# Kernel optimization log

Measured on AMD Instinct MI355X. Metric: run time of the kernel, lower is better.

## Reference

```python
import jax, jax.numpy as jnp
import numpy as np

K = 4            # number of modes (init kwarg)
ALPHA = 2000.0   # bandwidth constraint
TAU = 0.0        # dual ascent step (0 -> exact reconstruction slack)
N_ITERS = 20     # fixed ADMM iterations (orig: tol-based while loop, max 500)


def vmd_batch(x):
    # x: [B, C, T] float32 -> (u: [B, C, K, T], omega: [B, C, K])
    B, C, T = x.shape
    T2 = 2 * T
    half = T2 // 2
    # mirror extension (vmdpy): flip first half | signal | flip second half
    f = jnp.concatenate([x[..., :T // 2][..., ::-1], x, x[..., T // 2:][..., ::-1]], axis=-1)  # [B,C,T2]
    t = jnp.arange(1, T2 + 1, dtype=jnp.float32) / T2
    freqs = t - 0.5 - 1.0 / T2                       # [T2], centered frequency axis
    freqs_pos = freqs[half:]                          # [T], positive frequencies
    f_hat = jnp.fft.fftshift(jnp.fft.fft(f, axis=-1), axes=-1).astype(jnp.complex64)
    f_hat_plus = f_hat.at[..., :half].set(0.0)        # keep analytic (positive-freq) part
    # init=1: uniform initial center frequencies
    omega = jnp.broadcast_to((0.5 / K) * jnp.arange(K, dtype=jnp.float32), (B, C, K))
    u_hat = jnp.zeros((B, C, K, T2), dtype=jnp.complex64)
    lam = jnp.zeros((B, C, T2), dtype=jnp.complex64)  # dual variable lambda_hat

    def step(carry, _):
        u_hat, omega, lam = carry
        S = jnp.sum(u_hat, axis=2)                    # running sum of all modes [B,C,T2]
        new_u, new_w = [], []
        for k in range(K):                            # Gauss-Seidel sweep over K modes (K small, unrolled)
            S = S - u_hat[:, :, k]                    # sum of all other modes (updated ones included)
            denom = 1.0 + ALPHA * (freqs[None, None, :] - omega[:, :, k:k + 1]) ** 2
            uk = (f_hat_plus - S + lam / 2.0) / denom # Wiener-filter spectral update [B,C,T2]
            S = S + uk
            p = uk.real[..., half:] ** 2 + uk.imag[..., half:] ** 2  # power on positive freqs [B,C,T]
            wk = jnp.sum(freqs_pos * p, axis=-1) / jnp.sum(p, axis=-1)  # center-frequency re-estimate
            new_u.append(uk)
            new_w.append(wk)
        u_hat = jnp.stack(new_u, axis=2)
        omega = jnp.stack(new_w, axis=-1)
        lam = lam + TAU * (S - f_hat_plus)            # dual ascent (tau=0 -> no-op, kept for fidelity)
        return (u_hat, omega, lam), None

    (u_hat, omega, lam), _ = jax.lax.scan(step, (u_hat, omega, lam), None, length=N_ITERS)

    # reconstruct full conjugate-symmetric spectrum
    pos = u_hat[..., half:]                           # [B,C,K,T]
    full = jnp.zeros((B, C, K, T2), dtype=jnp.complex64)
    full = full.at[..., half:].set(pos)
    full = full.at[..., 1:half + 1].set(jnp.conj(pos)[..., ::-1])  # full[half-j] = conj(pos[j])
    full = full.at[..., 0].set(jnp.conj(full[..., -1]))
    u = jnp.real(jnp.fft.ifft(jnp.fft.ifftshift(full, axes=-1), axis=-1))  # [B,C,K,T2]
    u = u[..., T2 // 4: 3 * T2 // 4]                  # de-mirror: center T samples
    return u, omega


def setup_inputs() -> dict:
    key = jax.random.key(0)
    x = jax.random.normal(key, (16, 8192, 4), dtype=jnp.float32)  # [B, T, C]
    return {"x": x}


def reference(x):
    # module forward: permute [B,T,C] -> [B,C,T], run VMD, return u:[B,K,T,C], omega:[B,K]
    u, omega = vmd_batch(jnp.transpose(x, (0, 2, 1)))
    u = jnp.transpose(u, (0, 2, 3, 1))                # [B,K,T,C]
    omega_b = jnp.mean(omega, axis=1)                 # collapse channel dim -> [B,K]
    return (u, omega_b)
```

## Files before the change

### kernel.cpp

```cpp
#include <hip/hip_runtime.h>


#define HALF      8192
#define NH        8192
#define NTHREADS  1024
#define KMODES    4
#define NITERS    20
#define ALPHA_F   2000.0f
#define SQH       0.70710678118654752440f
#define SENTINEL  0xFFFFFFFFu

typedef __fp16 half2_t __attribute__((ext_vector_type(2)));
typedef float  v2f     __attribute__((ext_vector_type(2)));

__device__ __forceinline__ unsigned bitrev13(unsigned x) { return __brev(x) >> 19; }
__device__ __forceinline__ unsigned bitrev11(unsigned x) { return __brev(x) >> 21; }
__device__ __forceinline__ int pidx(int i) { return i + (i >> 4); }

__device__ __forceinline__ unsigned pack_h2(float a, float b) {
    half2_t h = __builtin_amdgcn_cvt_pkrtz(a, b);
    return __builtin_bit_cast(unsigned, h);
}
__device__ __forceinline__ v2f unpack_h2(unsigned u) {
    half2_t h = __builtin_bit_cast(half2_t, u);
    v2f r; r.x = (float)h.x; r.y = (float)h.y; return r;
}

__device__ __forceinline__ unsigned ic_load(const unsigned* p) {
    return __hip_atomic_load(p, __ATOMIC_RELAXED, __HIP_MEMORY_SCOPE_AGENT);
}
__device__ __forceinline__ void ic_store(unsigned* p, unsigned v) {
    __hip_atomic_store(p, v, __ATOMIC_RELAXED, __HIP_MEMORY_SCOPE_AGENT);
}
__device__ __forceinline__ unsigned long long ic_load64(const unsigned long long* p) {
    return __hip_atomic_load(p, __ATOMIC_RELAXED, __HIP_MEMORY_SCOPE_AGENT);
}
__device__ __forceinline__ void ic_store64(unsigned long long* p, unsigned long long v) {
    __hip_atomic_store(p, v, __ATOMIC_RELAXED, __HIP_MEMORY_SCOPE_AGENT);
}
__device__ __forceinline__ void store_plain(unsigned* p, unsigned v) {
    asm volatile("global_store_dword %0, %1, off" :: "v"(p), "v"(v) : "memory");
}
__device__ __forceinline__ unsigned load_sc0(const unsigned* p) {
    unsigned r;
    asm volatile("global_load_dword %0, %1, off sc0\n\t"
                 "s_waitcnt vmcnt(0)"
                 : "=v"(r) : "v"(p) : "memory");
    return r;
}

template <int CTRL>
__device__ __forceinline__ float dpp_add_step(float v) {
    int r = __builtin_amdgcn_update_dpp(0, __float_as_int(v), CTRL, 0xf, 0xf, true);
    return v + __int_as_float(r);
}
__device__ __forceinline__ float wave64_sum(float v) {
    v = dpp_add_step<0x111>(v);
    v = dpp_add_step<0x112>(v);
    v = dpp_add_step<0x114>(v);
    v = dpp_add_step<0x118>(v);
    v = dpp_add_step<0x142>(v);
    v = dpp_add_step<0x143>(v);
    return v;
}

__device__ __forceinline__ float2 cmul(float2 a, float wr, float wi) {
    return make_float2(a.x * wr - a.y * wi, a.x * wi + a.y * wr);
}
__device__ __forceinline__ float2 cadd(float2 a, float2 b) {
    return make_float2(a.x + b.x, a.y + b.y);
}
__device__ __forceinline__ float2 csub(float2 a, float2 b) {
    return make_float2(a.x - b.x, a.y - b.y);
}

template <bool INV>
__device__ __forceinline__ void fft_pass8_g(float2* A, int bf, int log2Q, float invL) {
    const int Q    = 1 << log2Q;
    const int j    = bf & (Q - 1);
    const int base = ((bf >> log2Q) << (log2Q + 3)) + j;

    float2 x[8];
    #pragma unroll
    for (int m = 0; m < 8; ++m) x[m] = A[pidx(base + m * Q)];

    float rev = (float)j * invL;
    float w1r = __builtin_amdgcn_cosf(rev);
    float w1i = INV ?  __builtin_amdgcn_sinf(rev)
                    : -__builtin_amdgcn_sinf(rev);
    float w2r = w1r * w1r - w1i * w1i, w2i = 2.0f * w1r * w1i;
    float w4r = w2r * w2r - w2i * w2i, w4i = 2.0f * w2r * w2i;
    float wsr, wsi;
    if (INV) { wsr = SQH * (w1r - w1i); wsi = SQH * (w1r + w1i); }
    else     { wsr = SQH * (w1r + w1i); wsi = SQH * (w1i - w1r); }
    float w1tr = INV ? -w1i : w1i,  w1ti = INV ? w1r : -w1r;
    float wstr = INV ? -wsi : wsi,  wsti = INV ? wsr : -wsr;
    float w2tr = INV ? -w2i : w2i,  w2ti = INV ? w2r : -w2r;

    float2 y0 = cadd(x[0], x[4]), y1 = cadd(x[1], x[5]);
    float2 y2 = cadd(x[2], x[6]), y3 = cadd(x[3], x[7]);
    float2 y4 = cmul(csub(x[0], x[4]), w1r, w1i);
    float2 y5 = cmul(csub(x[1], x[5]), wsr, wsi);
    float2 y6 = cmul(csub(x[2], x[6]), w1tr, w1ti);
    float2 y7 = cmul(csub(x[3], x[7]), wstr, wsti);

    float2 z0 = cadd(y0, y2), z2 = cmul(csub(y0, y2), w2r, w2i);
    float2 z1 = cadd(y1, y3), z3 = cmul(csub(y1, y3), w2tr, w2ti);
    float2 z4 = cadd(y4, y6), z6 = cmul(csub(y4, y6), w2r, w2i);
    float2 z5 = cadd(y5, y7), z7 = cmul(csub(y5, y7), w2tr, w2ti);

    A[pidx(base + 0 * Q)] = cadd(z0, z1);
    A[pidx(base + 1 * Q)] = cmul(csub(z0, z1), w4r, w4i);
    A[pidx(base + 2 * Q)] = cadd(z2, z3);
    A[pidx(base + 3 * Q)] = cmul(csub(z2, z3), w4r, w4i);
    A[pidx(base + 4 * Q)] = cadd(z4, z5);
    A[pidx(base + 5 * Q)] = cmul(csub(z4, z5), w4r, w4i);
    A[pidx(base + 6 * Q)] = cadd(z6, z7);
    A[pidx(base + 7 * Q)] = cmul(csub(z6, z7), w4r, w4i);
}
template <bool INV>
__device__ __forceinline__ void fft_pass8(float2* A, int tid, int t) {
    fft_pass8_g<INV>(A, tid, 10 - 3 * t, (float)(1 << (3 * t)) * (1.0f / 8192.0f));
}

__device__ __forceinline__ void fft_last2(float2* A, int tid) {
    #pragma unroll
    for (int u = 0; u < 4; ++u) {
        int t  = tid + u * NTHREADS;
        int i0 = 2 * t, i1 = 2 * t + 1;
        float2 a = A[pidx(i0)], b = A[pidx(i1)];
        A[pidx(i0)] = make_float2(a.x + b.x, a.y + b.y);
        A[pidx(i1)] = make_float2(a.x - b.x, a.y - b.y);
    }
}

__device__ __forceinline__ void fft2048_last4(float2* A, int g) {
    int i0 = 4 * g;
    float2 a0 = A[pidx(i0)], a1 = A[pidx(i0 + 1)];
    float2 a2 = A[pidx(i0 + 2)], a3 = A[pidx(i0 + 3)];
    float2 b0 = cadd(a0, a2), b1 = cadd(a1, a3);
    float2 b2 = csub(a0, a2);
    float2 d  = csub(a1, a3);
    float2 b3 = make_float2(d.y, -d.x);
    A[pidx(i0)]     = cadd(b0, b1);
    A[pidx(i0 + 1)] = csub(b0, b1);
    A[pidx(i0 + 2)] = cadd(b2, b3);
    A[pidx(i0 + 3)] = csub(b2, b3);
}

__device__ __forceinline__ int mirror_t(int i) {
    if (i < 4096)       return 4095 - i;
    else if (i < 12288) return i - 4096;
    else                return 20479 - i;
}

__global__ __launch_bounds__(NTHREADS) void vmd_fused(
    const float* __restrict__ x, unsigned* __restrict__ ws_u,
    unsigned* __restrict__ ws_omega, unsigned* __restrict__ ws_partf,
    unsigned* __restrict__ ws_parts, unsigned* __restrict__ ws_udone,
    unsigned* __restrict__ ws_yflag, unsigned long long* __restrict__ ws_Y,
    float* __restrict__ out)
{
    __shared__ float2 A[NH + (NH >> 4)];
    const int tid = threadIdx.x;
    const int bid = blockIdx.x;
    const int r8  = bid & 7;
    const int q   = (bid >> 3) & 3;
    const int a8  = bid >> 5;
    const int ch  = a8 * 8 + r8;
    const int b   = ch >> 2, c = ch & 3;
    const float* xb = x + (size_t)b * 8192 * 4 + c;

    for (int m = tid; m < 2048; m += NTHREADS) {
        int i0 = 8 * m + 2 * q;
        float re = xb[(size_t)mirror_t(i0) * 4];
        float im = xb[(size_t)mirror_t(i0 + 1) * 4];
        A[pidx(m)] = make_float2(re, im);
    }
    __syncthreads();
    for (int t = 0; t < 3; ++t) {
        if (tid < 256)
            fft_pass8_g<false>(A, tid, 8 - 3 * t,
                               (float)(1 << (3 * t)) * (1.0f / 2048.0f));
        __syncthreads();
    }
    if (tid < 512) fft2048_last4(A, tid);
    __syncthreads();

    float2 own0, own1;
    {
        unsigned long long* ydst = ws_Y + ((size_t)ch * 4 + q) * 2048;
        own0 = A[pidx((int)bitrev11((unsigned)tid))];
        own1 = A[pidx((int)bitrev11((unsigned)(tid + NTHREADS)))];
        ic_store64(ydst + tid,            __builtin_bit_cast(unsigned long long, own0));
        ic_store64(ydst + tid + NTHREADS, __builtin_bit_cast(unsigned long long, own1));
    }
    asm volatile("s_waitcnt vmcnt(0)" ::: "memory");
    __syncthreads();
    if (tid == 0) ic_store(ws_yflag + ch * 4 + q, 0u);
    if (tid < 4) {
        const unsigned* p = ws_yflag + ch * 4 + tid;
        for (;;) {
            unsigned w = ic_load(p);
            if (w != SENTINEL) break;
            __builtin_amdgcn_s_sleep(1);
        }
    }
    __syncthreads();

    {
        A[pidx((q << 11) + tid)]            = own0;
        A[pidx((q << 11) + tid + NTHREADS)] = own1;
        const unsigned long long* ysrc = ws_Y + (size_t)ch * 8192;
        unsigned long long yv[6];
        int ri[3], n = 0;
        #pragma unroll
        for (int r = 0; r < 4; ++r) if (r != q) ri[n++] = r;
        #pragma unroll
        for (int w = 0; w < 3; ++w) {
            yv[2 * w]     = ic_load64(ysrc + (ri[w] << 11) + tid);
            yv[2 * w + 1] = ic_load64(ysrc + (ri[w] << 11) + tid + NTHREADS);
        }
        #pragma unroll
        for (int w = 0; w < 3; ++w) {
            A[pidx((ri[w] << 11) + tid)]            = __builtin_bit_cast(float2, yv[2 * w]);
            A[pidx((ri[w] << 11) + tid + NTHREADS)] = __builtin_bit_cast(float2, yv[2 * w + 1]);
        }
    }
    __syncthreads();

    v2f R[2];
    #pragma unroll
    for (int u = 0; u < 2; ++u) {
        int jp  = tid + u * NTHREADS;
        int j   = (q << 11) + jp;
        int j2p = (2048 - jp) & 2047;
        float2 y0 = A[pidx(jp)];
        float2 y1 = A[pidx(2048 + jp)];
        float2 y2 = A[pidx(4096 + jp)];
        float2 y3 = A[pidx(6144 + jp)];
        float2 h0 = A[pidx(j2p)];
        float2 h1 = A[pidx(2048 + j2p)];
        float2 h2 = A[pidx(4096 + j2p)];
        float2 h3 = A[pidx(6144 + j2p)];
        float rev = (float)j * (1.0f / 8192.0f);
        float wr = __builtin_amdgcn_cosf(rev);
        float wi = -__builtin_amdgcn_sinf(rev);
        float w2r = wr * wr - wi * wi, w2i = 2.0f * wr * wi;
        float w3r = w2r * wr - w2i * wi, w3i = w2r * wi + w2i * wr;
        float2 zj = y0;
        zj.x += y1.x * wr  - y1.y * wi;  zj.y += y1.x * wi  + y1.y * wr;
        zj.x += y2.x * w2r - y2.y * w2i; zj.y += y2.x * w2i + y2.y * w2r;
        zj.x += y3.x * w3r - y3.y * w3i; zj.y += y3.x * w3i + y3.y * w3r;
        float2 zh = h0;
        zh.x += h1.x * wr  + h1.y * wi;  zh.y += -h1.x * wi  + h1.y * wr;
        zh.x += h2.x * w2r + h2.y * w2i; zh.y += -h2.x * w2i + h2.y * w2r;
        zh.x += h3.x * w3r + h3.y * w3i; zh.y += -h3.x * w3i + h3.y * w3r;
        float ex = 0.5f * (zj.x + zh.x);
        float ey = 0.5f * (zj.y - zh.y);
        float dx = 0.5f * (zj.x - zh.x);
        float dy = 0.5f * (zj.y + zh.y);
        float rev2 = (float)j * (1.0f / 16384.0f);
        float ur = __builtin_amdgcn_cosf(rev2);
        float ui = -__builtin_amdgcn_sinf(rev2);
        R[u].x = ex + ur * dy + ui * dx;
        R[u].y = ey + ui * dy - ur * dx;
    }
    __syncthreads();

    v2f Up[KMODES][2];
    #pragma unroll
    for (int u = 0; u < 2; ++u)
        #pragma unroll
        for (int k = 0; k < KMODES; ++k) { Up[k][u].x = 0.f; Up[k][u].y = 0.f; }

    const float f0 = (float)((q << 11) + tid) * (1.0f / 16384.0f);
    float omg[KMODES] = {0.0f, 0.125f, 0.25f, 0.375f};

    float* red = (float*)A;
    const int lane = tid & 63, wid = tid >> 6;

    for (int it = 0; it < NITERS; ++it) {
        v2f nd[KMODES];
        #pragma unroll
        for (int k = 0; k < KMODES; ++k) { nd[k].x = 0.f; nd[k].y = 0.f; }
        #pragma unroll
        for (int u = 0; u < 2; ++u) {
            const float fru = f0 + (float)u * 0.0625f;
            v2f fv; fv.x = fru; fv.y = 1.0f;
            #pragma unroll
            for (int k = 0; k < KMODES; ++k) {
                float d   = fru - omg[k];
                float dnm = fmaf(ALPHA_F * d, d, 1.0f);
                float rcp = __builtin_amdgcn_rcpf(dnm);
                v2f uo  = Up[k][u];
                v2f nm  = R[u] + uo;
                v2f un  = nm * rcp;
                R[u]    = nm - un;
                Up[k][u] = un;
                float p = fmaf(un.x, un.x, un.y * un.y);
                nd[k]   = fv * p + nd[k];
            }
        }
        float num[KMODES], den[KMODES];
        #pragma unroll
        for (int m = 0; m < KMODES; ++m) {
            num[m] = wave64_sum(nd[m].x);
            den[m] = wave64_sum(nd[m].y);
        }
        float* redb = red + (it & 1) * 144;
        if (lane == 63) {
            float4* r4 = (float4*)&redb[wid * 8];
            r4[0] = make_float4(num[0], num[1], num[2], num[3]);
            r4[1] = make_float4(den[0], den[1], den[2], den[3]);
        }
        __syncthreads();
        const bool last_it = (it == NITERS - 1);
        unsigned* ppf = ws_partf + (((size_t)it * 64 + ch) << 5);
        unsigned* pps = ws_parts + (((size_t)it * 64 + ch) << 5);
        if (wid == 0) {
            float v = redb[lane] + redb[lane + 64];
            v += __int_as_float(__builtin_amdgcn_ds_swizzle(__float_as_int(v), 0x201F));
            v += __int_as_float(__builtin_amdgcn_ds_swizzle(__float_as_int(v), 0x401F));
            v += __int_as_float(__builtin_amdgcn_ds_bpermute((lane ^ 32) << 2,
                                                             __float_as_int(v)));
            if (lane < 8) {
                unsigned bits = __float_as_uint(v);
                store_plain(ppf + (q << 3) + lane, bits);
                ic_store(pps + (q << 3) + lane, bits);
            }
            if (!last_it || q == 0) {
                float t = 0.0f;
                if (lane < 32) {
                    unsigned w;
                    for (;;) {
                        w = load_sc0(ppf + lane);
                        if (w != SENTINEL) break;
                        w = ic_load(pps + lane);
                        if (w != SENTINEL) break;
                        __builtin_amdgcn_s_sleep(1);
                    }
                    t = __uint_as_float(w);
                }
                t += __int_as_float(__builtin_amdgcn_ds_swizzle(__float_as_int(t), 0x201F));
                t += __int_as_float(__builtin_amdgcn_ds_swizzle(__float_as_int(t), 0x401F));
                if (!last_it) {
                    if (lane < 8) redb[128 + lane] = t;
                } else {
                    #pragma unroll
                    for (int m = 0; m < KMODES; ++m) {
                        float nm_ = __int_as_float(__builtin_amdgcn_readlane(__float_as_int(t), m));
                        float dn_ = __int_as_float(__builtin_amdgcn_readlane(__float_as_int(t), m + 4));
                        omg[m] = nm_ * __builtin_amdgcn_rcpf(dn_);
                    }
                }
            }
        }
        if (!last_it) {
            __syncthreads();
            #pragma unroll
            for (int m = 0; m < KMODES; ++m) {
                float nm_ = redb[128 + m];
                float dn_ = redb[128 + m + 4];
                omg[m] = nm_ * __builtin_amdgcn_rcpf(dn_);
            }
        }
    }

    #pragma unroll
    for (int k = 0; k < KMODES; ++k) {
        unsigned* dst = ws_u + (size_t)(ch * KMODES + k) * HALF + (q << 11);
        #pragma unroll
        for (int u = 0; u < 2; ++u)
            ic_store(dst + tid + u * NTHREADS, pack_h2(Up[k][u].x, Up[k][u].y));
    }
    if (q == 0 && tid < KMODES)
        ic_store(ws_omega + ch * KMODES + tid, __float_as_uint(omg[tid]));
    asm volatile("s_waitcnt vmcnt(0)" ::: "memory");
    __syncthreads();
    if (tid == 0)
        ic_store(ws_udone + (ch << 2) + q, 0u);

    const int s2  = bid & 7;
    const int c2  = (bid >> 3) & 3;
    const int a2  = bid >> 5;
    const int g2  = a2 * 8 + s2;
    const int b2  = g2 >> 2, k2 = g2 & 3;
    const int ch2 = b2 * 4 + c2;
    const unsigned* pos = ws_u + (size_t)(ch2 * KMODES + k2) * HALF;

    if (bid == 0 && tid < 64) {
        int bb = tid >> 2, kk = tid & 3;
        float s = 0.f;
        #pragma unroll
        for (int cc = 0; cc < 4; ++cc) {
            const unsigned* p = ws_omega + ((bb * 4 + cc) << 2) + kk;
            unsigned w;
            for (;;) {
                w = ic_load(p);
                if (w != SENTINEL) break;
                __builtin_amdgcn_s_sleep(1);
            }
            s += __uint_as_float(w);
        }
        out[2097152 + tid] = 0.25f * s;
    }

    if (tid < 4) {
        const unsigned* p = ws_udone + (ch2 << 2) + tid;
        for (;;) {
            unsigned w = ic_load(p);
            if (w != SENTINEL) break;
            __builtin_amdgcn_s_sleep(1);
        }
    }
    __syncthreads();

    {
        unsigned wj[8], wh[8];
        #pragma unroll
        for (int uu = 0; uu < 8; ++uu) {
            int j = tid + uu * NTHREADS;
            wj[uu] = ic_load(pos + j);
            wh[uu] = ic_load(pos + (j ? (HALF - j) : (HALF - 1)));
        }
        #pragma unroll
        for (int uu = 0; uu < 8; ++uu) {
            int j = tid + uu * NTHREADS;
            v2f pj = unpack_h2(wj[uu]);
            v2f ph = unpack_h2(wh[uu]);
            float gjx = pj.x, gjy = (j == 0) ? -pj.y : pj.y;
            float ghx = ph.x, ghy = -ph.y;
            float ex = 0.5f * (gjx + ghx), ey = 0.5f * (gjy + ghy);
            float dx = 0.5f * (gjx - ghx), dy = 0.5f * (gjy - ghy);
            float rev = (float)j * (1.0f / 16384.0f);
            float wr = __builtin_amdgcn_cosf(rev);
            float wi = __builtin_amdgcn_sinf(rev);
            float ox = dx * wr - dy * wi;
            float oy = dx * wi + dy * wr;
            A[pidx(j)] = make_float2(ex - oy, ey + ox);
        }
    }
    __syncthreads();

    for (int t = 0; t < 4; ++t) {
        fft_pass8<true>(A, tid, t);
        __syncthreads();
    }
    fft_last2(A, tid);
    __syncthreads();

    float* outp = out + (size_t)(b2 * 4 + k2) * 8192 * 4 + c2;
    for (int m = 2048 + tid; m < 6144; m += NTHREADS) {
        float2 z = A[pidx((int)bitrev13((unsigned)m))];
        int t0 = 2 * m - 4096;
        outp[(size_t)t0 * 4]       = z.x * (1.0f / 8192.0f);
        outp[(size_t)(t0 + 1) * 4] = z.y * (1.0f / 8192.0f);
    }
}

extern "C" void kernel_launch(void* const* d_in, const int* in_sizes, int n_in,
                              void* d_out, int out_size, void* d_ws, size_t ws_size,
                              hipStream_t stream)
{
    (void)in_sizes; (void)n_in; (void)out_size; (void)ws_size;
    const float* x = (const float*)d_in[0];
    float* out = (float*)d_out;

    unsigned* ws_u     = (unsigned*)d_ws;
    unsigned* ws_omega = (unsigned*)((char*)d_ws + (size_t)64 * 4 * HALF * 4);
    unsigned* ws_partf = ws_omega + 256;
    unsigned* ws_parts = ws_partf + (size_t)NITERS * 64 * 32;
    unsigned* ws_udone = ws_parts + (size_t)NITERS * 64 * 32;
    unsigned* ws_yflag = ws_udone + 256;
    unsigned long long* ws_Y = (unsigned long long*)(ws_yflag + 256);

    hipMemsetAsync(ws_omega, 0xFF,
                   (size_t)(256 + 2 * NITERS * 64 * 32 + 256 + 256) * 4, stream);
    vmd_fused<<<256, NTHREADS, 0, stream>>>(x, ws_u, ws_omega, ws_partf,
                                            ws_parts, ws_udone, ws_yflag,
                                            ws_Y, out);
}
```

Before: 79.82 us.

## Interleave two channels per block to hide cross-block omega reduction latency

Each block now owns one octant of frequency bins for two different channels (A and B, offset by four octants) rather than a quarter of one channel. The ADMM loop alternates between them, so the global gather of channel B's partial sums from the previous iteration overlaps with channel A's local compute, and the reverse. The aim is to hide the inter-block spin-wait latency that previously stalled every iteration. The cost is a second Y-load and combine pass, doubled partial-sum and flag workspace, and more complex synchronisation ordering.

```diff
diff --git a/kernel.cpp b/kernel.cpp
--- a/kernel.cpp
+++ b/kernel.cpp
@@ -62,6 +62,32 @@
     v = dpp_add_step<0x142>(v);
     v = dpp_add_step<0x143>(v);
     return v;
+}
+
+__device__ __forceinline__ float fold16x8(const float* slab, int lane) {
+    float v = slab[lane] + slab[lane + 64];
+    v += __int_as_float(__builtin_amdgcn_ds_swizzle(__float_as_int(v), 0x201F));
+    v += __int_as_float(__builtin_amdgcn_ds_swizzle(__float_as_int(v), 0x401F));
+    v += __int_as_float(__builtin_amdgcn_ds_bpermute((lane ^ 32) << 2,
+                                                     __float_as_int(v)));
+    return v;
+}
+__device__ __forceinline__ float gather_fold(const unsigned* basef,
+                                             const unsigned* bases, int lane) {
+    unsigned w;
+    for (;;) {
+        w = load_sc0(basef + lane);
+        if (w != SENTINEL) break;
+        w = ic_load(bases + lane);
+        if (w != SENTINEL) break;
+        __builtin_amdgcn_s_sleep(1);
+    }
+    float t = __uint_as_float(w);
+    t += __int_as_float(__builtin_amdgcn_ds_swizzle(__float_as_int(t), 0x201F));
+    t += __int_as_float(__builtin_amdgcn_ds_swizzle(__float_as_int(t), 0x401F));
+    t += __int_as_float(__builtin_amdgcn_ds_bpermute((lane ^ 32) << 2,
+                                                     __float_as_int(t)));
+    return t;
 }
 
 __device__ __forceinline__ float2 cmul(float2 a, float wr, float wi) {
@@ -154,6 +180,43 @@
     else                return 20479 - i;
 }
 
+__device__ __forceinline__ v2f combine_bin(const float2* A, int j) {
+    int jp  = j & 2047;
+    int j2p = (2048 - jp) & 2047;
+    float2 y0 = A[pidx(jp)];
+    float2 y1 = A[pidx(2048 + jp)];
+    float2 y2 = A[pidx(4096 + jp)];
+    float2 y3 = A[pidx(6144 + jp)];
+    float2 h0 = A[pidx(j2p)];
+    float2 h1 = A[pidx(2048 + j2p)];
+    float2 h2 = A[pidx(4096 + j2p)];
+    float2 h3 = A[pidx(6144 + j2p)];
+    float rev = (float)j * (1.0f / 8192.0f);
+    float wr = __builtin_amdgcn_cosf(rev);
+    float wi = -__builtin_amdgcn_sinf(rev);
+    float w2r = wr * wr - wi * wi, w2i = 2.0f * wr * wi;
+    float w3r = w2r * wr - w2i * wi, w3i = w2r * wi + w2i * wr;
+    float2 zj = y0;
+    zj.x += y1.x * wr  - y1.y * wi;  zj.y += y1.x * wi  + y1.y * wr;
+    zj.x += y2.x * w2r - y2.y * w2i; zj.y += y2.x * w2i + y2.y * w2r;
+    zj.x += y3.x * w3r - y3.y * w3i; zj.y += y3.x * w3i + y3.y * w3r;
+    float2 zh = h0;
+    zh.x += h1.x * wr  + h1.y * wi;  zh.y += -h1.x * wi  + h1.y * wr;
+    zh.x += h2.x * w2r + h2.y * w2i; zh.y += -h2.x * w2i + h2.y * w2r;
+    zh.x += h3.x * w3r + h3.y * w3i; zh.y += -h3.x * w3i + h3.y * w3r;
+    float ex = 0.5f * (zj.x + zh.x);
+    float ey = 0.5f * (zj.y - zh.y);
+    float dx = 0.5f * (zj.x - zh.x);
+    float dy = 0.5f * (zj.y + zh.y);
+    float rev2 = (float)j * (1.0f / 16384.0f);
+    float ur = __builtin_amdgcn_cosf(rev2);
+    float ui = -__builtin_amdgcn_sinf(rev2);
+    v2f R;
+    R.x = ex + ur * dy + ui * dx;
+    R.y = ey + ui * dy - ur * dx;
+    return R;
+}
+
 __global__ __launch_bounds__(NTHREADS) void vmd_fused(
     const float* __restrict__ x, unsigned* __restrict__ ws_u,
     unsigned* __restrict__ ws_omega, unsigned* __restrict__ ws_partf,
@@ -162,17 +225,17 @@
     float* __restrict__ out)
 {
     __shared__ float2 A[NH + (NH >> 4)];
-    const int tid = threadIdx.x;
-    const int bid = blockIdx.x;
-    const int r8  = bid & 7;
-    const int q   = (bid >> 3) & 3;
-    const int a8  = bid >> 5;
-    const int ch  = a8 * 8 + r8;
-    const int b   = ch >> 2, c = ch & 3;
-    const float* xb = x + (size_t)b * 8192 * 4 + c;
+    const int tid  = threadIdx.x;
+    const int bid  = blockIdx.x;
+    const int chA  = bid & 63;
+    const int octA = bid >> 6;
+    const int chB  = chA ^ 1;
+    const int octB = octA + 4;
+    const int bA   = chA >> 2, cA = chA & 3;
+    const float* xb = x + (size_t)bA * 8192 * 4 + cA;
 
     for (int m = tid; m < 2048; m += NTHREADS) {
-        int i0 = 8 * m + 2 * q;
+        int i0 = 8 * m + 2 * octA;
         float re = xb[(size_t)mirror_t(i0) * 4];
         float im = xb[(size_t)mirror_t(i0 + 1) * 4];
         A[pidx(m)] = make_float2(re, im);
@@ -189,7 +252,7 @@
 
     float2 own0, own1;
     {
-        unsigned long long* ydst = ws_Y + ((size_t)ch * 4 + q) * 2048;
+        unsigned long long* ydst = ws_Y + ((size_t)chA * 4 + octA) * 2048;
         own0 = A[pidx((int)bitrev11((unsigned)tid))];
         own1 = A[pidx((int)bitrev11((unsigned)(tid + NTHREADS)))];
         ic_store64(ydst + tid,            __builtin_bit_cast(unsigned long long, own0));
@@ -197,9 +260,9 @@
     }
     asm volatile("s_waitcnt vmcnt(0)" ::: "memory");
     __syncthreads();
-    if (tid == 0) ic_store(ws_yflag + ch * 4 + q, 0u);
+    if (tid == 0) ic_store(ws_yflag + chA * 4 + octA, 0u);
     if (tid < 4) {
-        const unsigned* p = ws_yflag + ch * 4 + tid;
+        const unsigned* p = ws_yflag + chA * 4 + tid;
         for (;;) {
             unsigned w = ic_load(p);
             if (w != SENTINEL) break;
@@ -207,15 +270,14 @@
         }
     }
     __syncthreads();
-
     {
-        A[pidx((q << 11) + tid)]            = own0;
-        A[pidx((q << 11) + tid + NTHREADS)] = own1;
-        const unsigned long long* ysrc = ws_Y + (size_t)ch * 8192;
+        A[pidx((octA << 11) + tid)]            = own0;
+        A[pidx((octA << 11) + tid + NTHREADS)] = own1;
+        const unsigned long long* ysrc = ws_Y + (size_t)chA * 8192;
         unsigned long long yv[6];
         int ri[3], n = 0;
         #pragma unroll
-        for (int r = 0; r < 4; ++r) if (r != q) ri[n++] = r;
+        for (int r = 0; r < 4; ++r) if (r != octA) ri[n++] = r;
         #pragma unroll
         for (int w = 0; w < 3; ++w) {
             yv[2 * w]     = ic_load64(ysrc + (ri[w] << 11) + tid);
@@ -228,130 +290,156 @@
         }
     }
     __syncthreads();
-
-    v2f R[2];
+    v2f RA = combine_bin(A, (octA << 10) + tid);
+    __syncthreads();
+
+    if (tid < 4) {
+        const unsigned* p = ws_yflag + chB * 4 + tid;
+        for (;;) {
+            unsigned w = ic_load(p);
+            if (w != SENTINEL) break;
+            __builtin_amdgcn_s_sleep(1);
+        }
+    }
+    __syncthreads();
+    {
+        const unsigned long long* ysrc = ws_Y + (size_t)chB * 8192;
+        unsigned long long yv[8];
+        #pragma unroll
+        for (int r = 0; r < 4; ++r) {
+            yv[2 * r]     = ic_load64(ysrc + (r << 11) + tid);
+            yv[2 * r + 1] = ic_load64(ysrc + (r << 11) + tid + NTHREADS);
+        }
+        #pragma unroll
+        for (int r = 0; r < 4; ++r) {
+            A[pidx((r << 11) + tid)]            = __builtin_bit_cast(float2, yv[2 * r]);
+            A[pidx((r << 11) + tid + NTHREADS)] = __builtin_bit_cast(float2, yv[2 * r + 1]);
+        }
+    }
+    __syncthreads();
+    v2f RB = combine_bin(A, (octB << 10) + tid);
+    __syncthreads();
+
+    v2f UpA[KMODES], UpB[KMODES];
     #pragma unroll
-    for (int u = 0; u < 2; ++u) {
-        int jp  = tid + u * NTHREADS;
-        int j   = (q << 11) + jp;
-        int j2p = (2048 - jp) & 2047;
-        float2 y0 = A[pidx(jp)];
-        float2 y1 = A[pidx(2048 + jp)];
-        float2 y2 = A[pidx(4096 + jp)];
-        float2 y3 = A[pidx(6144 + jp)];
-        float2 h0 = A[pidx(j2p)];
-        float2 h1 = A[pidx(2048 + j2p)];
-        float2 h2 = A[pidx(4096 + j2p)];
-        float2 h3 = A[pidx(6144 + j2p)];
-        float rev = (float)j * (1.0f / 8192.0f);
-        float wr = __builtin_amdgcn_cosf(rev);
-        float wi = -__builtin_amdgcn_sinf(rev);
-        float w2r = wr * wr - wi * wi, w2i = 2.0f * wr * wi;
-        float w3r = w2r * wr - w2i * wi, w3i = w2r * wi + w2i * wr;
-        float2 zj = y0;
-        zj.x += y1.x * wr  - y1.y * wi;  zj.y += y1.x * wi  + y1.y * wr;
-        zj.x += y2.x * w2r - y2.y * w2i; zj.y += y2.x * w2i + y2.y * w2r;
-        zj.x += y3.x * w3r - y3.y * w3i; zj.y += y3.x * w3i + y3.y * w3r;
-        float2 zh = h0;
-        zh.x += h1.x * wr  + h1.y * wi;  zh.y += -h1.x * wi  + h1.y * wr;
-        zh.x += h2.x * w2r + h2.y * w2i; zh.y += -h2.x * w2i + h2.y * w2r;
-        zh.x += h3.x * w3r + h3.y * w3i; zh.y += -h3.x * w3i + h3.y * w3r;
-        float ex = 0.5f * (zj.x + zh.x);
-        float ey = 0.5f * (zj.y - zh.y);
-        float dx = 0.5f * (zj.x - zh.x);
-        float dy = 0.5f * (zj.y + zh.y);
-        float rev2 = (float)j * (1.0f / 16384.0f);
-        float ur = __builtin_amdgcn_cosf(rev2);
-        float ui = -__builtin_amdgcn_sinf(rev2);
-        R[u].x = ex + ur * dy + ui * dx;
-        R[u].y = ey + ui * dy - ur * dx;
-    }
-    __syncthreads();
-
-    v2f Up[KMODES][2];
-    #pragma unroll
-    for (int u = 0; u < 2; ++u)
-        #pragma unroll
-        for (int k = 0; k < KMODES; ++k) { Up[k][u].x = 0.f; Up[k][u].y = 0.f; }
-
-    const float f0 = (float)((q << 11) + tid) * (1.0f / 16384.0f);
-    float omg[KMODES] = {0.0f, 0.125f, 0.25f, 0.375f};
-
-    float* red = (float*)A;
+    for (int k = 0; k < KMODES; ++k) {
+        UpA[k].x = 0.f; UpA[k].y = 0.f;
+        UpB[k].x = 0.f; UpB[k].y = 0.f;
+    }
+    float omgA[KMODES] = {0.0f, 0.125f, 0.25f, 0.375f};
+    float omgB[KMODES] = {0.0f, 0.125f, 0.25f, 0.375f};
+    const float fA = (float)((octA << 10) + tid) * (1.0f / 16384.0f);
+    const float fB = (float)((octB << 10) + tid) * (1.0f / 16384.0f);
+
+    float* slabA  = (float*)A;
+    float* oslabA = slabA + 128;
+    float* slabB  = slabA + 136;
+    float* oslabB = slabA + 264;
     const int lane = tid & 63, wid = tid >> 6;
 
     for (int it = 0; it < NITERS; ++it) {
-        v2f nd[KMODES];
-        #pragma unroll
-        for (int k = 0; k < KMODES; ++k) { nd[k].x = 0.f; nd[k].y = 0.f; }
-        #pragma unroll
-        for (int u = 0; u < 2; ++u) {
-            const float fru = f0 + (float)u * 0.0625f;
-            v2f fv; fv.x = fru; fv.y = 1.0f;
+        const bool last_it = (it == NITERS - 1);
+        {
+            v2f nd[KMODES];
+            #pragma unroll
+            for (int k = 0; k < KMODES; ++k) { nd[k].x = 0.f; nd[k].y = 0.f; }
+            v2f fv; fv.x = fA; fv.y = 1.0f;
             #pragma unroll
             for (int k = 0; k < KMODES; ++k) {
-                float d   = fru - omg[k];
+                float d   = fA - omgA[k];
                 float dnm = fmaf(ALPHA_F * d, d, 1.0f);
                 float rcp = __builtin_amdgcn_rcpf(dnm);
-                v2f uo  = Up[k][u];
-                v2f nm  = R[u] + uo;
-                v2f un  = nm * rcp;
-                R[u]    = nm - un;
-                Up[k][u] = un;
+                v2f nm = RA + UpA[k];
+                v2f un = nm * rcp;
+                RA = nm - un;
+                UpA[k] = un;
                 float p = fmaf(un.x, un.x, un.y * un.y);
-                nd[k]   = fv * p + nd[k];
-            }
-        }
-        float num[KMODES], den[KMODES];
-        #pragma unroll
-        for (int m = 0; m < KMODES; ++m) {
-            num[m] = wave64_sum(nd[m].x);
-            den[m] = wave64_sum(nd[m].y);
-        }
-        float* redb = red + (it & 1) * 144;
-        if (lane == 63) {
-            float4* r4 = (float4*)&redb[wid * 8];
-            r4[0] = make_float4(num[0], num[1], num[2], num[3]);
-            r4[1] = make_float4(den[0], den[1], den[2], den[3]);
+                nd[k] = fv * p + nd[k];
+            }
+            float num[KMODES], den[KMODES];
+            #pragma unroll
+            for (int m = 0; m < KMODES; ++m) {
+                num[m] = wave64_sum(nd[m].x);
+                den[m] = wave64_sum(nd[m].y);
+            }
+            if (lane == 63) {
+                float4* r4 = (float4*)&slabA[wid * 8];
+                r4[0] = make_float4(num[0], num[1], num[2], num[3]);
+                r4[1] = make_float4(den[0], den[1], den[2], den[3]);
+            }
         }
         __syncthreads();
-        const bool last_it = (it == NITERS - 1);
-        unsigned* ppf = ws_partf + (((size_t)it * 64 + ch) << 5);
-        unsigned* pps = ws_parts + (((size_t)it * 64 + ch) << 5);
+        unsigned* pAf = ws_partf + (((size_t)it * 64 + chA) << 6);
+        unsigned* pAs = ws_parts + (((size_t)it * 64 + chA) << 6);
         if (wid == 0) {
-            float v = redb[lane] + redb[lane + 64];
-            v += __int_as_float(__builtin_amdgcn_ds_swizzle(__float_as_int(v), 0x201F));
-            v += __int_as_float(__builtin_amdgcn_ds_swizzle(__float_as_int(v), 0x401F));
-            v += __int_as_float(__builtin_amdgcn_ds_bpermute((lane ^ 32) << 2,
-                                                             __float_as_int(v)));
+            float v = fold16x8(slabA, lane);
             if (lane < 8) {
                 unsigned bits = __float_as_uint(v);
-                store_plain(ppf + (q << 3) + lane, bits);
-                ic_store(pps + (q << 3) + lane, bits);
-            }
-            if (!last_it || q == 0) {
-                float t = 0.0f;
-                if (lane < 32) {
-                    unsigned w;
-                    for (;;) {
-                        w = load_sc0(ppf + lane);
-                        if (w != SENTINEL) break;
-                        w = ic_load(pps + lane);
-                        if (w != SENTINEL) break;
-                        __builtin_amdgcn_s_sleep(1);
-                    }
-                    t = __uint_as_float(w);
-                }
-                t += __int_as_float(__builtin_amdgcn_ds_swizzle(__float_as_int(t), 0x201F));
-                t += __int_as_float(__builtin_amdgcn_ds_swizzle(__float_as_int(t), 0x401F));
+                store_plain(pAf + (octA << 3) + lane, bits);
+                ic_store(pAs + (octA << 3) + lane, bits);
+            }
+            if (it > 0) {
+                unsigned* qf = ws_partf + (((size_t)(it - 1) * 64 + chB) << 6);
+                unsigned* qs = ws_parts + (((size_t)(it - 1) * 64 + chB) << 6);
+                float t = gather_fold(qf, qs, lane);
+                if (lane < 8) oslabB[lane] = t;
+            }
+        }
+        __syncthreads();
+        if (it > 0) {
+            #pragma unroll
+            for (int m = 0; m < KMODES; ++m)
+                omgB[m] = oslabB[m] * __builtin_amdgcn_rcpf(oslabB[m + 4]);
+        }
+        {
+            v2f nd[KMODES];
+            #pragma unroll
+            for (int k = 0; k < KMODES; ++k) { nd[k].x = 0.f; nd[k].y = 0.f; }
+            v2f fv; fv.x = fB; fv.y = 1.0f;
+            #pragma unroll
+            for (int k = 0; k < KMODES; ++k) {
+                float d   = fB - omgB[k];
+                float dnm = fmaf(ALPHA_F * d, d, 1.0f);
+                float rcp = __builtin_amdgcn_rcpf(dnm);
+                v2f nm = RB + UpB[k];
+                v2f un = nm * rcp;
+                RB = nm - un;
+                UpB[k] = un;
+                float p = fmaf(un.x, un.x, un.y * un.y);
+                nd[k] = fv * p + nd[k];
+            }
+            float num[KMODES], den[KMODES];
+            #pragma unroll
+            for (int m = 0; m < KMODES; ++m) {
+                num[m] = wave64_sum(nd[m].x);
+                den[m] = wave64_sum(nd[m].y);
+            }
+            if (lane == 63) {
+                float4* r4 = (float4*)&slabB[wid * 8];
+                r4[0] = make_float4(num[0], num[1], num[2], num[3]);
+                r4[1] = make_float4(den[0], den[1], den[2], den[3]);
+            }
+        }
+        __syncthreads();
+        unsigned* pBf = ws_partf + (((size_t)it * 64 + chB) << 6);
+        unsigned* pBs = ws_parts + (((size_t)it * 64 + chB) << 6);
+        if (wid == 0) {
+            float v = fold16x8(slabB, lane);
+            if (lane < 8) {
+                unsigned bits = __float_as_uint(v);
+                store_plain(pBf + (octB << 3) + lane, bits);
+                ic_store(pBs + (octB << 3) + lane, bits);
+            }
+            if (!last_it || octA == 0) {
+                float t = gather_fold(pAf, pAs, lane);
                 if (!last_it) {
-                    if (lane < 8) redb[128 + lane] = t;
+                    if (lane < 8) oslabA[lane] = t;
                 } else {
                     #pragma unroll
                     for (int m = 0; m < KMODES; ++m) {
                         float nm_ = __int_as_float(__builtin_amdgcn_readlane(__float_as_int(t), m));
                         float dn_ = __int_as_float(__builtin_amdgcn_readlane(__float_as_int(t), m + 4));
-                        omg[m] = nm_ * __builtin_amdgcn_rcpf(dn_);
+                        omgA[m] = nm_ * __builtin_amdgcn_rcpf(dn_);
                     }
                 }
             }
@@ -359,27 +447,26 @@
         if (!last_it) {
             __syncthreads();
             #pragma unroll
-            for (int m = 0; m < KMODES; ++m) {
-                float nm_ = redb[128 + m];
-                float dn_ = redb[128 + m + 4];
-                omg[m] = nm_ * __builtin_amdgcn_rcpf(dn_);
-            }
+            for (int m = 0; m < KMODES; ++m)
+                omgA[m] = oslabA[m] * __builtin_amdgcn_rcpf(oslabA[m + 4]);
         }
     }
 
     #pragma unroll
     for (int k = 0; k < KMODES; ++k) {
-        unsigned* dst = ws_u + (size_t)(ch * KMODES + k) * HALF + (q << 11);
-        #pragma unroll
-        for (int u = 0; u < 2; ++u)
-            ic_store(dst + tid + u * NTHREADS, pack_h2(Up[k][u].x, Up[k][u].y));
-    }
-    if (q == 0 && tid < KMODES)
-        ic_store(ws_omega + ch * KMODES + tid, __float_as_uint(omg[tid]));
+        ic_store(ws_u + (size_t)(chA * KMODES + k) * HALF + (octA << 10) + tid,
+                 pack_h2(UpA[k].x, UpA[k].y));
+        ic_store(ws_u + (size_t)(chB * KMODES + k) * HALF + (octB << 10) + tid,
+                 pack_h2(UpB[k].x, UpB[k].y));
+    }
+    if (octA == 0 && tid < KMODES)
+        ic_store(ws_omega + chA * KMODES + tid, __float_as_uint(omgA[tid]));
     asm volatile("s_waitcnt vmcnt(0)" ::: "memory");
     __syncthreads();
-    if (tid == 0)
-        ic_store(ws_udone + (ch << 2) + q, 0u);
+    if (tid == 0) {
+        ic_store(ws_udone + (chA << 3) + octA, 0u);
+        ic_store(ws_udone + (chB << 3) + octB, 0u);
+    }
 
     const int s2  = bid & 7;
     const int c2  = (bid >> 3) & 3;
@@ -406,8 +493,8 @@
         out[2097152 + tid] = 0.25f * s;
     }
 
-    if (tid < 4) {
-        const unsigned* p = ws_udone + (ch2 << 2) + tid;
+    if (tid < 8) {
+        const unsigned* p = ws_udone + (ch2 << 3) + tid;
         for (;;) {
             unsigned w = ic_load(p);
             if (w != SENTINEL) break;
@@ -470,13 +557,13 @@
     unsigned* ws_u     = (unsigned*)d_ws;
     unsigned* ws_omega = (unsigned*)((char*)d_ws + (size_t)64 * 4 * HALF * 4);
     unsigned* ws_partf = ws_omega + 256;
-    unsigned* ws_parts = ws_partf + (size_t)NITERS * 64 * 32;
-    unsigned* ws_udone = ws_parts + (size_t)NITERS * 64 * 32;
-    unsigned* ws_yflag = ws_udone + 256;
+    unsigned* ws_parts = ws_partf + (size_t)NITERS * 64 * 64;
+    unsigned* ws_udone = ws_parts + (size_t)NITERS * 64 * 64;
+    unsigned* ws_yflag = ws_udone + 512;
     unsigned long long* ws_Y = (unsigned long long*)(ws_yflag + 256);
 
     hipMemsetAsync(ws_omega, 0xFF,
-                   (size_t)(256 + 2 * NITERS * 64 * 32 + 256 + 256) * 4, stream);
+                   (size_t)(256 + 2 * NITERS * 64 * 64 + 512 + 256) * 4, stream);
     vmd_fused<<<256, NTHREADS, 0, stream>>>(x, ws_u, ws_omega, ws_partf,
                                             ws_parts, ws_udone, ws_yflag,
                                             ws_Y, out);
```

New measurement: 142.6 us. 78.6% more time.
